# Performance work log

Measured on AMD Instinct MI355X. Metric: run time of the kernel, lower is better.

## Reference

```python
import jax, jax.numpy as jnp
import numpy as np

B, N, C, S = 4, 200000, 96, 32
EPS = 1e-05


def setup_inputs() -> dict:
    key = jax.random.key(0)
    kx, kw, kb = jax.random.split(key, 3)
    x = jax.random.normal(kx, (B, N, C), dtype=jnp.float32)
    # Build mutually-consistent CSR offsets (non-empty segments) and per-point segment ids.
    rng = np.random.default_rng(0)
    cuts = np.sort(rng.choice(np.arange(1, N), size=S - 1, replace=False))
    offsets = np.concatenate([[0], cuts, [N]]).astype(np.int64)  # [S+1]
    indices = np.repeat(np.arange(S, dtype=np.int64), np.diff(offsets))  # [N]
    weight = 1.0 + 0.1 * jax.random.normal(kw, (C,), dtype=jnp.float32)
    bias = 0.1 * jax.random.normal(kb, (C,), dtype=jnp.float32)
    return {
        "x": x,
        "batch_offsets": jnp.asarray(offsets),
        "batch_indices": jnp.asarray(indices),
        "weight": weight,
        "bias": bias,
    }


def reference(x, batch_offsets, batch_indices, weight, bias):
    # x: [B, N, C]; batch_offsets: [S+1]; batch_indices: [N]
    counts = (batch_offsets[1:] - batch_offsets[:-1]).astype(x.dtype)  # [S]
    n_seg = counts.shape[0]
    # per-point mean over channels -> segment mean over points (segment_csr 'mean')
    mx = jnp.mean(x, axis=-1)  # [B, N]
    seg_mean = jnp.zeros((x.shape[0], n_seg), x.dtype).at[:, batch_indices].add(mx) / counts  # [B, S]
    nx = x - seg_mean[:, batch_indices, None]  # [B, N, C]
    n2 = jnp.mean(nx * nx, axis=-1)  # [B, N]
    seg_var = jnp.zeros((x.shape[0], n_seg), x.dtype).at[:, batch_indices].add(n2) / counts  # [B, S]
    std = jnp.sqrt(seg_var + EPS)  # [B, S]
    return nx / std[:, batch_indices, None] * weight + bias
```

## Files before the change

### kernel.cpp

```cpp
#include <hip/hip_runtime.h>

#define B_      4
#define N_      200000
#define C_      96
#define S_      32
#define EPS_    1e-5f

#define C4      (C_ / 4)
#define NC4     (N_ * C4)
#define THREADS 256
#define ITER    30
#define CHUNK   (THREADS * ITER)
#define GRIDX   (NC4 / CHUNK)
#define GROUPS  (ITER / 3)

typedef float f32x4 __attribute__((ext_vector_type(4)));

__device__ __forceinline__ float4 scale4(const float4 a, const float s) {
    return make_float4(a.x * s, a.y * s, a.z * s, a.w * s);
}
__device__ __forceinline__ float4 nms4(const float4 bb, const float m, const float4 fw) {
    return make_float4(bb.x - m * fw.x, bb.y - m * fw.y, bb.z - m * fw.z, bb.w - m * fw.w);
}

__global__ __launch_bounds__(THREADS) void stats_kernel(
    const float4* __restrict__ x,
    const int*    __restrict__ offsets,
    float*        __restrict__ gsum,
    float*        __restrict__ gsq)
{
    __shared__ int   soff[S_ + 1];
    __shared__ float lsum[S_];
    __shared__ float lsq [S_];
    const int t = threadIdx.x;
    if (t <= S_) soff[t] = offsets[t];
    if (t <  S_) { lsum[t] = 0.f; lsq[t] = 0.f; }
    __syncthreads();

    const int b = blockIdx.y;
    const float4* xb = x + (size_t)b * NC4;
    const int f0 = blockIdx.x * CHUNK + t;

    int n = f0 / 24;
    int c = f0 - n * 24;
    int sg = 0;
    #pragma unroll
    for (int st = 16; st; st >>= 1) {
        const int cand = sg + st;
        if (soff[cand] <= n) sg = cand;
    }
    int nxt = soff[sg + 1];

    float s1 = 0.f, s2 = 0.f;
    for (int k = 0; k < ITER; ++k) {
        if (n >= nxt) {
            atomicAdd(&lsum[sg], s1);
            atomicAdd(&lsq [sg], s2);
            s1 = 0.f; s2 = 0.f;
            do { ++sg; } while (soff[sg + 1] <= n);
            nxt = soff[sg + 1];
        }
        const float4 v = xb[f0 + k * THREADS];
        s1 += (v.x + v.y) + (v.z + v.w);
        s2 += v.x * v.x + v.y * v.y + v.z * v.z + v.w * v.w;
        c += 16; if (c >= 24) { c -= 24; ++n; }
        n += 10;
    }
    atomicAdd(&lsum[sg], s1);
    atomicAdd(&lsq [sg], s2);
    __syncthreads();

    if (t < S_) {
        const float a = lsum[t];
        const float q = lsq[t];
        if (a != 0.f || q != 0.f) {
            atomicAdd(&gsum[b * S_ + t], a);
            atomicAdd(&gsq [b * S_ + t], q);
        }
    }
}

__global__ void finalize_kernel(
    const float* __restrict__ gsum,
    const float* __restrict__ gsq,
    const int*   __restrict__ offsets,
    float*       __restrict__ mean,
    float*       __restrict__ rstd)
{
    const int i = threadIdx.x;
    if (i < B_ * S_) {
        const int s = i % S_;
        const float cnt = (float)(offsets[s + 1] - offsets[s]) * (float)C_;
        const float m = gsum[i] / cnt;
        const float v = gsq[i] / cnt - m * m;
        mean[i] = m;
        rstd[i] = rsqrtf(fmaxf(v, 0.f) + EPS_);
    }
}

__global__ __launch_bounds__(THREADS) void norm_kernel(
    const float4* __restrict__ x,
    const int*    __restrict__ offsets,
    const float4* __restrict__ wgt,
    const float4* __restrict__ bia,
    const float*  __restrict__ mean,
    const float*  __restrict__ rstd,
    float4*       __restrict__ out)
{
    __shared__ int    soff[S_ + 1];
    __shared__ float4 lw[C4];
    __shared__ float4 lb[C4];
    __shared__ float  lm[S_];
    __shared__ float  lr[S_];
    const int t = threadIdx.x;
    const int b = blockIdx.y;
    if (t <= S_) soff[t] = offsets[t];
    if (t <  C4) { lw[t] = wgt[t]; lb[t] = bia[t]; }
    if (t <  S_) { lm[t] = mean[b * S_ + t]; lr[t] = rstd[b * S_ + t]; }
    __syncthreads();

    const float4* xb = x   + (size_t)b * NC4;
    float4*       ob = out + (size_t)b * NC4;
    const int f0 = blockIdx.x * CHUNK + t;

    const int c0 = f0 - (f0 / 24) * 24;
    int c1 = c0 + 16; if (c1 >= 24) c1 -= 24;
    int c2 = c0 + 8;  if (c2 >= 24) c2 -= 24;

    const int fhi = f0 + (ITER - 1) * THREADS;
    int n = fhi / 24;
    int c = fhi - n * 24;

    int sg = 0;
    #pragma unroll
    for (int st = 16; st; st >>= 1) {
        const int cand = sg + st;
        if (soff[cand] <= n) sg = cand;
    }
    int lo = soff[sg];

    float4 fw0, fb0, fw1, fb1, fw2, fb2;
#define RECOMP() { \
        const float m_ = lm[sg], r_ = lr[sg]; \
        fw0 = scale4(lw[c0], r_); fb0 = nms4(lb[c0], m_, fw0); \
        fw1 = scale4(lw[c1], r_); fb1 = nms4(lb[c1], m_, fw1); \
        fw2 = scale4(lw[c2], r_); fb2 = nms4(lb[c2], m_, fw2); \
    }
    RECOMP();

#define NBODY(K, J) { \
        if (n < lo) {                                    \
            do { --sg; } while (n < soff[sg]);           \
            lo = soff[sg]; \
            RECOMP(); \
        } \
        const int fi = f0 + (K) * THREADS; \
        const float4 v = xb[fi]; \
        float4 o; \
        o.x = v.x * fw##J.x + fb##J.x; \
        o.y = v.y * fw##J.y + fb##J.y; \
        o.z = v.z * fw##J.z + fb##J.z; \
        o.w = v.w * fw##J.w + fb##J.w; \
        __builtin_nontemporal_store(*(const f32x4*)&o, (f32x4*)(ob + fi)); \
        c -= 16; if (c < 0) { c += 24; --n; } \
        n -= 10; \
    }

    for (int g = GROUPS - 1; g >= 0; --g) {
        NBODY(3 * g + 2, 2)
        NBODY(3 * g + 1, 1)
        NBODY(3 * g + 0, 0)
    }
#undef NBODY
#undef RECOMP
}

extern "C" void kernel_launch(void* const* d_in, const int* in_sizes, int n_in,
                              void* d_out, int out_size, void* d_ws, size_t ws_size,
                              hipStream_t stream)
{
    const float* x       = (const float*)d_in[0];
    const int*   offsets = (const int*)  d_in[1];
    const int*   indices = (const int*)  d_in[2];
    const float* weight  = (const float*)d_in[3];
    const float* bias    = (const float*)d_in[4];
    float*       out     = (float*)d_out;
    (void)indices; (void)in_sizes; (void)n_in; (void)out_size; (void)ws_size;

    float* gsum = (float*)d_ws;
    float* gsq  = gsum + B_ * S_;
    float* mean = gsq  + B_ * S_;
    float* rstd = mean + B_ * S_;

    hipMemsetAsync(d_ws, 0, 2 * B_ * S_ * sizeof(float), stream);

    dim3 grid(GRIDX, B_);
    stats_kernel<<<grid, THREADS, 0, stream>>>(
        (const float4*)x, offsets, gsum, gsq);

    finalize_kernel<<<1, 128, 0, stream>>>(gsum, gsq, offsets, mean, rstd);

    norm_kernel<<<grid, THREADS, 0, stream>>>(
        (const float4*)x, offsets, (const float4*)weight, (const float4*)bias,
        mean, rstd, (float4*)out);
}
```

Measured before the change: 571.5 us.

## Fuse stats, finalize and normalize into one kernel with a grid barrier

Merges the statistics, finalize and normalization kernels into one persistent kernel. Blocks synchronize through a global atomic-counter barrier, then each block computes mean and rstd locally and normalizes its own chunk. Per-block work grows so the grid can fit co-resident. This removes two kernel launches and the intermediate mean/rstd buffers, and the chunk re-read may be served from cache. The spin barrier risks deadlock if not all blocks are resident, and blocks sit idle while waiting.

```diff
diff --git a/kernel.cpp b/kernel.cpp
--- a/kernel.cpp
+++ b/kernel.cpp
@@ -9,9 +9,10 @@
 #define C4      (C_ / 4)
 #define NC4     (N_ * C4)
 #define THREADS 256
-#define ITER    30
+#define ITER    75
 #define CHUNK   (THREADS * ITER)
-#define GRIDX   (NC4 / CHUNK)
+#define BLK_X   (NC4 / CHUNK)
+#define NBLK    (BLK_X * B_)
 #define GROUPS  (ITER / 3)
 
 typedef float f32x4 __attribute__((ext_vector_type(4)));
@@ -23,26 +24,36 @@
     return make_float4(bb.x - m * fw.x, bb.y - m * fw.y, bb.z - m * fw.z, bb.w - m * fw.w);
 }
 
-__global__ __launch_bounds__(THREADS) void stats_kernel(
+__global__ __launch_bounds__(THREADS, 4) void fused_kernel(
     const float4* __restrict__ x,
     const int*    __restrict__ offsets,
+    const float4* __restrict__ wgt,
+    const float4* __restrict__ bia,
     float*        __restrict__ gsum,
-    float*        __restrict__ gsq)
+    float*        __restrict__ gsq,
+    int*          __restrict__ cnt,
+    float4*       __restrict__ out)
 {
-    __shared__ int   soff[S_ + 1];
-    __shared__ float lsum[S_];
-    __shared__ float lsq [S_];
+    __shared__ int    soff[S_ + 1];
+    __shared__ float  lsum[S_], lsq[S_];
+    __shared__ float4 lw[C4], lb[C4];
+    __shared__ float  lm[S_], lr[S_];
+
     const int t = threadIdx.x;
+    const int b = blockIdx.y;
+
     if (t <= S_) soff[t] = offsets[t];
     if (t <  S_) { lsum[t] = 0.f; lsq[t] = 0.f; }
+    if (t <  C4) { lw[t] = wgt[t]; lb[t] = bia[t]; }
     __syncthreads();
 
-    const int b = blockIdx.y;
     const float4* xb = x + (size_t)b * NC4;
     const int f0 = blockIdx.x * CHUNK + t;
 
     int n = f0 / 24;
-    int c = f0 - n * 24;
+    const int cstart = f0 - n * 24;
+    int c = cstart;
+
     int sg = 0;
     #pragma unroll
     for (int st = 16; st; st >>= 1) {
@@ -78,60 +89,37 @@
             atomicAdd(&gsq [b * S_ + t], q);
         }
     }
-}
 
-__global__ void finalize_kernel(
-    const float* __restrict__ gsum,
-    const float* __restrict__ gsq,
-    const int*   __restrict__ offsets,
-    float*       __restrict__ mean,
-    float*       __restrict__ rstd)
-{
-    const int i = threadIdx.x;
-    if (i < B_ * S_) {
-        const int s = i % S_;
-        const float cnt = (float)(offsets[s + 1] - offsets[s]) * (float)C_;
-        const float m = gsum[i] / cnt;
-        const float v = gsq[i] / cnt - m * m;
-        mean[i] = m;
-        rstd[i] = rsqrtf(fmaxf(v, 0.f) + EPS_);
+    __syncthreads();
+    if (t == 0) {
+        __threadfence();
+        atomicAdd(cnt, 1);
+        while (atomicAdd(cnt, 0) < NBLK) __builtin_amdgcn_s_sleep(16);
     }
-}
-
-__global__ __launch_bounds__(THREADS) void norm_kernel(
-    const float4* __restrict__ x,
-    const int*    __restrict__ offsets,
-    const float4* __restrict__ wgt,
-    const float4* __restrict__ bia,
-    const float*  __restrict__ mean,
-    const float*  __restrict__ rstd,
-    float4*       __restrict__ out)
-{
-    __shared__ int    soff[S_ + 1];
-    __shared__ float4 lw[C4];
-    __shared__ float4 lb[C4];
-    __shared__ float  lm[S_];
-    __shared__ float  lr[S_];
-    const int t = threadIdx.x;
-    const int b = blockIdx.y;
-    if (t <= S_) soff[t] = offsets[t];
-    if (t <  C4) { lw[t] = wgt[t]; lb[t] = bia[t]; }
-    if (t <  S_) { lm[t] = mean[b * S_ + t]; lr[t] = rstd[b * S_ + t]; }
     __syncthreads();
 
-    const float4* xb = x   + (size_t)b * NC4;
-    float4*       ob = out + (size_t)b * NC4;
-    const int f0 = blockIdx.x * CHUNK + t;
+    if (t < S_) {
+        const float s1g = atomicAdd(&gsum[b * S_ + t], 0.f);
+        const float s2g = atomicAdd(&gsq [b * S_ + t], 0.f);
+        const float cf  = (float)(soff[t + 1] - soff[t]) * (float)C_;
+        const float m   = s1g / cf;
+        const float v   = s2g / cf - m * m;
+        lm[t] = m;
+        lr[t] = rsqrtf(fmaxf(v, 0.f) + EPS_);
+    }
+    __syncthreads();
 
-    const int c0 = f0 - (f0 / 24) * 24;
+    float4* ob = out + (size_t)b * NC4;
+
+    const int c0 = cstart;
     int c1 = c0 + 16; if (c1 >= 24) c1 -= 24;
     int c2 = c0 + 8;  if (c2 >= 24) c2 -= 24;
 
     const int fhi = f0 + (ITER - 1) * THREADS;
-    int n = fhi / 24;
-    int c = fhi - n * 24;
+    n = fhi / 24;
+    c = fhi - n * 24;
 
-    int sg = 0;
+    sg = 0;
     #pragma unroll
     for (int st = 16; st; st >>= 1) {
         const int cand = sg + st;
@@ -189,18 +177,12 @@
 
     float* gsum = (float*)d_ws;
     float* gsq  = gsum + B_ * S_;
-    float* mean = gsq  + B_ * S_;
-    float* rstd = mean + B_ * S_;
+    int*   cnt  = (int*)(gsq + B_ * S_);
 
-    hipMemsetAsync(d_ws, 0, 2 * B_ * S_ * sizeof(float), stream);
+    hipMemsetAsync(d_ws, 0, (2 * B_ * S_ + 1) * sizeof(float), stream);
 
-    dim3 grid(GRIDX, B_);
-    stats_kernel<<<grid, THREADS, 0, stream>>>(
-        (const float4*)x, offsets, gsum, gsq);
-
-    finalize_kernel<<<1, 128, 0, stream>>>(gsum, gsq, offsets, mean, rstd);
-
-    norm_kernel<<<grid, THREADS, 0, stream>>>(
+    dim3 grid(BLK_X, B_);
+    fused_kernel<<<grid, THREADS, 0, stream>>>(
         (const float4*)x, offsets, (const float4*)weight, (const float4*)bias,
-        mean, rstd, (float4*)out);
+        gsum, gsq, cnt, (float4*)out);
 }
```

Result: slower. 662.8 us (+16.0%).
